# Optimization experiments

Measured on AMD Instinct MI355X. Metric: run time of the kernel, lower is better.

Reference implementation:

```python
import jax, jax.numpy as jnp
import numpy as np

H = 128        # hidden_size
V = 100000     # item vocab
B = 1024       # sessions
NODES = 32     # unique nodes per session (sections)
ITEMS = 16     # itemsets per session (sequence_len)
P = 8          # PADDED_LENGTH
N = B * NODES  # total nodes
T = B * ITEMS  # total itemsets


def setup_inputs() -> dict:
    key = jax.random.key(0)
    ks = jax.random.split(key, 10)
    s = 1.0 / np.sqrt(H)
    node_embedding = jax.random.normal(ks[0], (N, H), jnp.float32)
    emb_weight = jax.random.normal(ks[1], (V, H), jnp.float32) * s
    W1_w = jax.random.normal(ks[2], (H, H), jnp.float32) * s
    W1_b = jnp.zeros((H,), jnp.float32)
    W2_w = jax.random.normal(ks[3], (H, H), jnp.float32) * s
    W2_b = jnp.zeros((H,), jnp.float32)
    q_w = jax.random.normal(ks[4], (1, H), jnp.float32) * s
    q_b = jnp.zeros((1,), jnp.float32)
    W3_w = jax.random.normal(ks[5], (H, 2 * H), jnp.float32) * s
    W3_b = jnp.zeros((H,), jnp.float32)
    batch = jnp.repeat(jnp.arange(B, dtype=jnp.int32), NODES)  # sorted segment ids
    # local node indices per itemset; value == NODES means padding (zero row)
    sequence = jax.random.randint(ks[6], (T, P), 0, NODES + 1, jnp.int32)
    sequence = sequence.at[:, 0].set(jnp.minimum(sequence[:, 0], NODES - 1))  # >=1 valid entry
    itemset_len = jnp.sum(sequence < NODES, axis=1).astype(jnp.int32)
    sequence_len = jnp.full((B,), ITEMS, jnp.int32)
    cue = jax.random.randint(ks[7], (B,), 0, V, jnp.int32)
    return dict(node_embedding=node_embedding, emb_weight=emb_weight,
                W1_w=W1_w, W1_b=W1_b, W2_w=W2_w, W2_b=W2_b,
                q_w=q_w, q_b=q_b, W3_w=W3_w, W3_b=W3_b,
                batch=batch, sequence=sequence, itemset_len=itemset_len,
                sequence_len=sequence_len, cue=cue)


def reference(node_embedding, emb_weight, W1_w, W1_b, W2_w, W2_b,
              q_w, q_b, W3_w, W3_b, batch, sequence, itemset_len,
              sequence_len, cue):
    nB = sequence_len.shape[0]
    nN = node_embedding.shape[0]
    nT = sequence.shape[0]
    # per-session node counts (torch.bincount) and exclusive offsets (torch.split)
    sections = jax.ops.segment_sum(jnp.ones_like(batch), batch, num_segments=nB)
    node_off = jnp.cumsum(sections) - sections                      # [B]
    # session id of each itemset (torch.split(sequence, sequence_len))
    seq_cum = jnp.cumsum(sequence_len)                              # [B]
    itemset_seg = jnp.searchsorted(seq_cum, jnp.arange(nT), side='right')  # [T]
    # gather: local index == sections[s] hits the appended zero row -> mask to 0
    sec_t = sections[itemset_seg][:, None]                          # [T,1]
    valid = sequence < sec_t                                        # [T,P]
    gidx = jnp.clip(node_off[itemset_seg][:, None] + sequence, 0, nN - 1)
    gathered = jnp.where(valid[..., None], node_embedding[gidx], 0.0)  # [T,P,H]
    itemset_emb = gathered.sum(axis=1) / itemset_len[:, None].astype(node_embedding.dtype)  # [T,H]
    # last itemset of each session = v_n
    v_n = itemset_emb[seq_cum - 1]                                  # [B,H]
    v_n_rep = v_n[itemset_seg]                                      # [T,H]
    gate = jax.nn.sigmoid(v_n_rep @ W1_w.T + W1_b + itemset_emb @ W2_w.T + W2_b)
    alpha = gate @ q_w.T + q_b                                      # [T,1]
    s_g = jax.ops.segment_sum(alpha * itemset_emb, itemset_seg, num_segments=nB)  # [B,H]
    s_h = jnp.concatenate([v_n, s_g], axis=1) @ W3_w.T + W3_b       # [B,H]
    y_hat = jnp.sum(s_h * emb_weight[cue], axis=1)                  # [B]
    all_scores = s_h @ emb_weight.T                                 # [B,V]
    return (y_hat, all_scores)
```

## Files before the change

### kernel.cpp

```cpp
#include <hip/hip_runtime.h>
#include <hip/hip_bf16.h>

#define H 128
#define VOCAB 100000
#define B_SESS 1024
#define NODES 32
#define ITEMS 16
#define PADLEN 8

typedef short short8 __attribute__((ext_vector_type(8)));
typedef float f32x16 __attribute__((ext_vector_type(16)));
typedef float f32x4 __attribute__((ext_vector_type(4)));

static __device__ __forceinline__ short f2bf(float x) {
    unsigned u = __builtin_bit_cast(unsigned, x);
    u += 0x7fffu + ((u >> 16) & 1u);
    return (short)(u >> 16);
}

__global__ __launch_bounds__(256) void k_transpose(
    const float* __restrict__ W1, const float* __restrict__ W2,
    const float* __restrict__ W3,
    float* __restrict__ W1t, float* __restrict__ W2t, float* __restrict__ W3t)
{
    const int idx = blockIdx.x * 256 + threadIdx.x;
    const int k = idx >> 7, j = idx & 127;
    W1t[idx] = W1[j * H + k];
    W2t[idx] = W2[j * H + k];
    W3t[k * H + j]       = W3[j * 2 * H + k];
    W3t[(k + H) * H + j] = W3[j * 2 * H + k + H];
}

__global__ __launch_bounds__(H) void k_session(
    const float* __restrict__ node_emb,
    const int* __restrict__ sequence,
    const int* __restrict__ itemset_len,
    const float* __restrict__ W1t, const float* __restrict__ W1_b,
    const float* __restrict__ W2t, const float* __restrict__ W2_b,
    const float* __restrict__ q_w,  const float* __restrict__ q_b,
    const float* __restrict__ W3t, const float* __restrict__ W3_b,
    const float* __restrict__ emb_weight, const int* __restrict__ cue,
    float* __restrict__ y_hat, short* __restrict__ packA)
{
    __shared__ float it[ITEMS][H];
    __shared__ float contrib[ITEMS][H];
    __shared__ float red[ITEMS][8];
    __shared__ float alphas[ITEMS];
    __shared__ float sg[H];
    __shared__ float wred[2];

    const int b = blockIdx.x;
    const int j = threadIdx.x;
    const int nbase = b * NODES;

#pragma unroll
    for (int t = 0; t < ITEMS; ++t) {
        const int tg = b * ITEMS + t;
        float acc = 0.f;
#pragma unroll
        for (int p = 0; p < PADLEN; ++p) {
            int s = sequence[tg * PADLEN + p];
            if (s < NODES) acc += node_emb[(nbase + s) * H + j];
        }
        it[t][j] = acc / (float)itemset_len[tg];
    }
    __syncthreads();

    float pre = W1_b[j] + W2_b[j];
#pragma unroll 4
    for (int k = 0; k < H; k += 4) {
        float4 v = *(const float4*)&it[ITEMS - 1][k];
        pre += W1t[(k + 0) * H + j] * v.x + W1t[(k + 1) * H + j] * v.y
             + W1t[(k + 2) * H + j] * v.z + W1t[(k + 3) * H + j] * v.w;
    }

    float h2[ITEMS];
#pragma unroll
    for (int t = 0; t < ITEMS; ++t) h2[t] = 0.f;
    for (int k = 0; k < H; k += 4) {
        float w0 = W2t[(k + 0) * H + j];
        float w1 = W2t[(k + 1) * H + j];
        float w2 = W2t[(k + 2) * H + j];
        float w3 = W2t[(k + 3) * H + j];
#pragma unroll
        for (int t = 0; t < ITEMS; ++t) {
            float4 v = *(const float4*)&it[t][k];
            h2[t] += w0 * v.x + w1 * v.y + w2 * v.z + w3 * v.w;
        }
    }

    const float qwj = q_w[j];
#pragma unroll
    for (int t = 0; t < ITEMS; ++t) {
        float g = 1.f / (1.f + __expf(-(pre + h2[t])));
        contrib[t][j] = qwj * g;
    }
    __syncthreads();

    {
        int t = j >> 3, part = j & 7;
        float s = 0.f;
#pragma unroll
        for (int u = 0; u < 16; ++u) s += contrib[t][part * 16 + u];
        red[t][part] = s;
    }
    __syncthreads();
    if (j < ITEMS) {
        float s = q_b[0];
#pragma unroll
        for (int u = 0; u < 8; ++u) s += red[j][u];
        alphas[j] = s;
    }
    __syncthreads();

    float sgj = 0.f;
#pragma unroll
    for (int t = 0; t < ITEMS; ++t) sgj += alphas[t] * it[t][j];
    sg[j] = sgj;
    __syncthreads();

    float sh = W3_b[j];
#pragma unroll 4
    for (int k = 0; k < H; k += 4) {
        float4 v = *(const float4*)&it[ITEMS - 1][k];
        sh += W3t[(k + 0) * H + j] * v.x + W3t[(k + 1) * H + j] * v.y
            + W3t[(k + 2) * H + j] * v.z + W3t[(k + 3) * H + j] * v.w;
    }
#pragma unroll 4
    for (int k = 0; k < H; k += 4) {
        float4 v = *(const float4*)&sg[k];
        sh += W3t[(H + k + 0) * H + j] * v.x + W3t[(H + k + 1) * H + j] * v.y
            + W3t[(H + k + 2) * H + j] * v.z + W3t[(H + k + 3) * H + j] * v.w;
    }

    {
        const int c = b >> 5, cl = b & 31;
        const int s = j >> 4, hi = (j >> 3) & 1, i = j & 7;
        packA[c * 4096 + s * 512 + hi * 256 + cl * 8 + i] = f2bf(sh);
    }

    float prod = sh * emb_weight[(long)cue[b] * H + j];
#pragma unroll
    for (int off = 32; off > 0; off >>= 1) prod += __shfl_down(prod, off);
    if ((j & 63) == 0) wred[j >> 6] = prod;
    __syncthreads();
    if (j == 0) y_hat[b] = wred[0] + wred[1];
}

__global__ __launch_bounds__(256, 4) void k_scores(
    const float* __restrict__ emb_weight,
    const short* __restrict__ packA,
    float* __restrict__ scores)
{
    const int nwg = 782;
    const int xcd = blockIdx.x & 7;
    const int idx = blockIdx.x >> 3;
    const int q = nwg >> 3, r = nwg & 7;
    const int bid = (xcd < r) ? (xcd * (q + 1) + idx)
                              : (r * (q + 1) + (xcd - r) * q + idx);

    const int wave = threadIdx.x >> 6;
    const int lane = threadIdx.x & 63;
    const int hi = lane >> 5;
    const int cl = lane & 31;
    const int col = bid * 128 + wave * 32 + cl;
    const bool valid = col < VOCAB;

    short8 bfrag[8];
    if (valid) {
        const float* row = emb_weight + (long)col * H;
#pragma unroll
        for (int s = 0; s < 8; ++s) {
            const f32x4* p = (const f32x4*)(row + s * 16 + hi * 8);
            f32x4 x = __builtin_nontemporal_load(p);
            f32x4 y = __builtin_nontemporal_load(p + 1);
            short8 f;
            f[0] = f2bf(x[0]); f[1] = f2bf(x[1]); f[2] = f2bf(x[2]); f[3] = f2bf(x[3]);
            f[4] = f2bf(y[0]); f[5] = f2bf(y[1]); f[6] = f2bf(y[2]); f[7] = f2bf(y[3]);
            bfrag[s] = f;
        }
    } else {
#pragma unroll
        for (int s = 0; s < 8; ++s) {
            short8 z;
#pragma unroll
            for (int i = 0; i < 8; ++i) z[i] = 0;
            bfrag[s] = z;
        }
    }

    for (int c = 0; c < B_SESS / 32; ++c) {
        const short* ap = packA + c * 4096 + hi * 256 + cl * 8;
        short8 a[8];
#pragma unroll
        for (int s = 0; s < 8; ++s) a[s] = *(const short8*)(ap + s * 512);
        f32x16 acc;
#pragma unroll
        for (int r2 = 0; r2 < 16; ++r2) acc[r2] = 0.f;
#pragma unroll
        for (int s = 0; s < 8; ++s)
            acc = __builtin_amdgcn_mfma_f32_32x32x16_bf16(a[s], bfrag[s], acc, 0, 0, 0);
        if (valid) {
            const int M0 = c * 32;
#pragma unroll
            for (int r2 = 0; r2 < 16; ++r2) {
                int rowm = (r2 & 3) + 8 * (r2 >> 2) + 4 * hi;
                __builtin_nontemporal_store(acc[r2],
                    &scores[(long)(M0 + rowm) * VOCAB + col]);
            }
        }
    }
}

extern "C" void kernel_launch(void* const* d_in, const int* in_sizes, int n_in,
                              void* d_out, int out_size, void* d_ws, size_t ws_size,
                              hipStream_t stream) {
    const float* node_emb   = (const float*)d_in[0];
    const float* emb_w      = (const float*)d_in[1];
    const float* W1_w       = (const float*)d_in[2];
    const float* W1_b       = (const float*)d_in[3];
    const float* W2_w       = (const float*)d_in[4];
    const float* W2_b       = (const float*)d_in[5];
    const float* q_w        = (const float*)d_in[6];
    const float* q_b        = (const float*)d_in[7];
    const float* W3_w       = (const float*)d_in[8];
    const float* W3_b       = (const float*)d_in[9];
    const int* sequence     = (const int*)d_in[11];
    const int* itemset_len  = (const int*)d_in[12];
    const int* cue          = (const int*)d_in[14];

    float* out    = (float*)d_out;
    float* y_hat  = out;
    float* scores = out + B_SESS;

    short* packA = (short*)d_ws;
    float* W1t   = (float*)((char*)d_ws + (256 << 10));
    float* W2t   = W1t + H * H;
    float* W3t   = W2t + H * H;

    k_transpose<<<64, 256, 0, stream>>>(W1_w, W2_w, W3_w, W1t, W2t, W3t);
    k_session<<<B_SESS, H, 0, stream>>>(node_emb, sequence, itemset_len,
                                        W1t, W1_b, W2t, W2_b,
                                        q_w, q_b, W3t, W3_b, emb_w, cue,
                                        y_hat, packA);
    const int nblk = (VOCAB + 127) / 128;
    k_scores<<<nblk, 256, 0, stream>>>(emb_w, packA, scores);
}
```

Measured before the change: 154.6 us.

## Stage packed session operand into double-buffered LDS via global_load_lds

The score kernel stops having every wave load the packed bf16 session matrix from global memory. Instead, each 32-row chunk is copied once per workgroup into a double-buffered LDS tile using direct global-to-LDS loads, and the next chunk is prefetched while the current MFMAs run. This cuts redundant L2 reads of the A operand by sharing it across the four waves. In exchange it adds a barrier per chunk, and the occupancy hint is raised from 4 to 8 workgroups per CU. The waitcnt accounting relies on the outstanding nontemporal stores being counted alongside the loads.

```diff
diff --git a/kernel.cpp b/kernel.cpp
--- a/kernel.cpp
+++ b/kernel.cpp
@@ -7,6 +7,7 @@
 #define NODES 32
 #define ITEMS 16
 #define PADLEN 8
+#define NCHUNK 32
 
 typedef short short8 __attribute__((ext_vector_type(8)));
 typedef float f32x16 __attribute__((ext_vector_type(16)));
@@ -147,11 +148,13 @@
     if (j == 0) y_hat[b] = wred[0] + wred[1];
 }
 
-__global__ __launch_bounds__(256, 4) void k_scores(
+__global__ __launch_bounds__(256, 8) void k_scores(
     const float* __restrict__ emb_weight,
     const short* __restrict__ packA,
     float* __restrict__ scores)
 {
+    __shared__ short lds_pack[2][4096];
+
     const int nwg = 782;
     const int xcd = blockIdx.x & 7;
     const int idx = blockIdx.x >> 3;
@@ -189,17 +192,37 @@
         }
     }
 
-    for (int c = 0; c < B_SESS / 32; ++c) {
-        const short* ap = packA + c * 4096 + hi * 256 + cl * 8;
-        short8 a[8];
-#pragma unroll
-        for (int s = 0; s < 8; ++s) a[s] = *(const short8*)(ap + s * 512);
+#define STAGE(cc, buf)                                                        \
+    {                                                                         \
+        const short* g0 = packA + (cc) * 4096 + wave * 1024 + lane * 8;       \
+        __builtin_amdgcn_global_load_lds(                                     \
+            (const __attribute__((address_space(1))) void*)g0,                \
+            (__attribute__((address_space(3))) void*)&lds_pack[buf][wave * 1024], \
+            16, 0, 0);                                                        \
+        __builtin_amdgcn_global_load_lds(                                     \
+            (const __attribute__((address_space(1))) void*)(g0 + 512),        \
+            (__attribute__((address_space(3))) void*)&lds_pack[buf][wave * 1024 + 512], \
+            16, 0, 0);                                                        \
+    }
+
+    STAGE(0, 0);
+    asm volatile("s_waitcnt vmcnt(0)" ::: "memory");
+    __builtin_amdgcn_s_barrier();
+
+    const int lbase = hi * 256 + cl * 8;
+
+    for (int c = 0; c < NCHUNK; ++c) {
+        const int cur = c & 1;
+        if (c + 1 < NCHUNK) STAGE(c + 1, cur ^ 1);
+
         f32x16 acc;
 #pragma unroll
         for (int r2 = 0; r2 < 16; ++r2) acc[r2] = 0.f;
 #pragma unroll
-        for (int s = 0; s < 8; ++s)
-            acc = __builtin_amdgcn_mfma_f32_32x32x16_bf16(a[s], bfrag[s], acc, 0, 0, 0);
+        for (int s = 0; s < 8; ++s) {
+            short8 a = *(const short8*)&lds_pack[cur][lbase + s * 512];
+            acc = __builtin_amdgcn_mfma_f32_32x32x16_bf16(a, bfrag[s], acc, 0, 0, 0);
+        }
         if (valid) {
             const int M0 = c * 32;
 #pragma unroll
@@ -209,7 +232,10 @@
                     &scores[(long)(M0 + rowm) * VOCAB + col]);
             }
         }
-    }
+        asm volatile("s_waitcnt vmcnt(16)" ::: "memory");
+        __builtin_amdgcn_s_barrier();
+    }
+#undef STAGE
 }
 
 extern "C" void kernel_launch(void* const* d_in, const int* in_sizes, int n_in,
```

Result: slower. 168.3 us (+8.8%).
